# Performance work log

Measured on AMD Instinct MI355X. Metric: run time of the kernel, lower is better.

The kernel has to match this reference:

```python
import jax, jax.numpy as jnp
import numpy as np

N, D, DH, H = 2048, 256, 256, 4
DHEAD = DH // H
NEG = -1e30


def setup_inputs() -> dict:
    key = jax.random.key(0)
    ks = jax.random.split(key, 24)
    s = 0.05
    inp = {
        'axiom_states': jax.random.normal(ks[0], (N, D), jnp.float32),
        'adj0': (jax.random.uniform(ks[1], (N, N)) < 0.015).astype(jnp.float32),
        'adj1': (jax.random.uniform(ks[2], (N, N)) < 0.015).astype(jnp.float32),
        'w0': jax.random.uniform(ks[3], (N, N), jnp.float32),
        'w1': jax.random.uniform(ks[4], (N, N), jnp.float32),
        'Wm0': jax.random.normal(ks[5], (DH, D), jnp.float32) * s,
        'bm0': jax.random.normal(ks[6], (DH,), jnp.float32) * s,
        'Wa0': jax.random.normal(ks[7], (H, 2 * D), jnp.float32) * s,
        'ba0': jax.random.normal(ks[8], (H,), jnp.float32) * s,
        'Wm1': jax.random.normal(ks[9], (DH, D), jnp.float32) * s,
        'bm1': jax.random.normal(ks[10], (DH,), jnp.float32) * s,
        'Wa1': jax.random.normal(ks[11], (H, 2 * D), jnp.float32) * s,
        'ba1': jax.random.normal(ks[12], (H,), jnp.float32) * s,
        'gru_wih': jax.random.normal(ks[13], (3 * D, 2 * DH), jnp.float32) * s,
        'gru_whh': jax.random.normal(ks[14], (3 * D, D), jnp.float32) * s,
        'gru_bih': jax.random.normal(ks[15], (3 * D,), jnp.float32) * s,
        'gru_bhh': jax.random.normal(ks[16], (3 * D,), jnp.float32) * s,
        'ln_g': jnp.ones((D,), jnp.float32),
        'ln_b': jnp.zeros((D,), jnp.float32),
    }
    return inp


def _edge_messages(x, adj, w, Wm, bm, Wa, ba):
    # GAT-style decomposition of Linear([x_i, x_j]) -> a_cur[i] + a_nb[j] + b
    a_cur = x @ Wa[:, :D].T                      # [N,H] (target i, first half of concat)
    a_nb = x @ Wa[:, D:].T                       # [N,H] (neighbor j, second half)
    s = a_nb[:, None, :] + a_cur[None, :, :] + ba  # [j,i,H]
    s = jax.nn.leaky_relu(s, 0.2)
    s = s * w[:, :, None]                        # edge-weight scaled scores (pre-softmax)
    mask = adj != 0                              # edge j -> i iff adj[j,i] != 0
    logits = jnp.where(mask[:, :, None], s, NEG)
    attn = jax.nn.softmax(logits, axis=0) * mask[:, :, None]  # zero for isolated nodes
    msg = (x @ Wm.T + bm).reshape(N, H, DHEAD)   # per-neighbor messages
    agg = jnp.einsum('jih,jhd->ihd', attn, msg)  # softmax-weighted sum over neighbors
    return agg.reshape(N, DH)


def _forward(axiom_states, adj0, adj1, w0, w1, Wm0, bm0, Wa0, ba0,
             Wm1, bm1, Wa1, ba1, gru_wih, gru_whh, gru_bih, gru_bhh, ln_g, ln_b):
    m0 = _edge_messages(axiom_states, adj0, w0, Wm0, bm0, Wa0, ba0)
    m1 = _edge_messages(axiom_states, adj1, w1, Wm1, bm1, Wa1, ba1)
    msg = jnp.concatenate([m0, m1], axis=-1)     # dropout is identity in eval
    # GRUCell (torch semantics)
    gi = msg @ gru_wih.T + gru_bih
    gh = axiom_states @ gru_whh.T + gru_bhh
    r = jax.nn.sigmoid(gi[:, :D] + gh[:, :D])
    z = jax.nn.sigmoid(gi[:, D:2 * D] + gh[:, D:2 * D])
    n = jnp.tanh(gi[:, 2 * D:] + r * gh[:, 2 * D:])
    h = (1.0 - z) * n + z * axiom_states
    # LayerNorm
    mu = jnp.mean(h, axis=-1, keepdims=True)
    var = jnp.var(h, axis=-1, keepdims=True)
    return (h - mu) * jax.lax.rsqrt(var + 1e-5) * ln_g + ln_b


def reference(axiom_states, adj0, adj1, w0, w1, Wm0, bm0, Wa0, ba0,
              Wm1, bm1, Wa1, ba1, gru_wih, gru_whh, gru_bih, gru_bhh, ln_g, ln_b):
    return _forward(axiom_states, adj0, adj1, w0, w1, Wm0, bm0, Wa0, ba0,
                    Wm1, bm1, Wa1, ba1, gru_wih, gru_whh, gru_bih, gru_bhh, ln_g, ln_b)
```

## Files before the change

kernel.cpp:

```cpp
#include <hip/hip_runtime.h>

#define NN 2048
#define DD 256
#define HH 4
#define PW 1280
#define ECAP 128

typedef unsigned short ushort_t;
typedef __attribute__((ext_vector_type(4))) unsigned short us4;
typedef __attribute__((ext_vector_type(8))) short s8;
typedef __attribute__((ext_vector_type(4))) float f4;

__device__ __forceinline__ ushort_t f2b(float f) {
    unsigned int u = __float_as_uint(f);
    return (ushort_t)((u + 0x7fffu + ((u >> 16) & 1u)) >> 16);
}
__device__ __forceinline__ float b2f(ushort_t b) {
    return __uint_as_float(((unsigned int)b) << 16);
}
__device__ __forceinline__ void gl_lds16(const void* g, void* l) {
    __builtin_amdgcn_global_load_lds(
        (const __attribute__((address_space(1))) void*)g,
        (__attribute__((address_space(3))) void*)l, 16, 0, 0);
}

#define P_XC  512
#define P_WC  832
#define P_WI  1216
#define P_NB  1344

__global__ __launch_bounds__(256) void prep_kernel(
    const float* __restrict__ x,
    const float* __restrict__ Wm0, const float* __restrict__ Wm1,
    const float* __restrict__ whh, const float* __restrict__ wih,
    const float* __restrict__ Wa0, const float* __restrict__ Wa1,
    ushort_t* __restrict__ xb, ushort_t* __restrict__ Wcatb, ushort_t* __restrict__ wihb,
    float* __restrict__ acur, float* __restrict__ anb)
{
    __shared__ float sh[16][257];
    const int b = blockIdx.x, t = threadIdx.x;

    if (b < P_XC) {
        const int id = b * 1024 + t * 4;
        const float4 v = *(const float4*)(x + id);
        us4 o; o.x = f2b(v.x); o.y = f2b(v.y); o.z = f2b(v.z); o.w = f2b(v.w);
        *(us4*)(xb + id) = o;
        return;
    }
    if (b < P_WC) {
        const int id = (b - P_XC) * 1024 + t * 4;
        const int c = id >> 8, k = id & 255;
        const float* src = (c < 256) ? Wm0 + (size_t)c * DD + k
                         : (c < 512) ? Wm1 + (size_t)(c - 256) * DD + k
                                     : whh + (size_t)(c - 512) * DD + k;
        const float4 v = *(const float4*)src;
        us4 o; o.x = f2b(v.x); o.y = f2b(v.y); o.z = f2b(v.z); o.w = f2b(v.w);
        *(us4*)(Wcatb + id) = o;
        return;
    }
    if (b < P_WI) {
        const int id = (b - P_WC) * 1024 + t * 4;
        const float4 v = *(const float4*)(wih + id);
        us4 o; o.x = f2b(v.x); o.y = f2b(v.y); o.z = f2b(v.z); o.w = f2b(v.w);
        *(us4*)(wihb + id) = o;
        return;
    }
    {
        const int i0 = (b - P_WI) * 16;
        for (int rr = 0; rr < 16; ++rr)
            sh[rr][t] = x[(size_t)(i0 + rr) * DD + t];
        __syncthreads();
        const int r = t >> 4, idx = t & 15;
        const int l = idx >> 3, isnb = (idx >> 2) & 1, h = idx & 3;
        const float* wrow = (l ? Wa1 : Wa0) + h * (2 * DD) + isnb * DD;
        float acc = 0.f;
        for (int k = 0; k < DD; ++k) acc = fmaf(sh[r][k], wrow[k], acc);
        float* dst = isnb ? anb : acur;
        dst[((size_t)l * NN + i0 + r) * HH + h] = acc;
    }
}

__device__ __forceinline__ void gemm_core(
    const ushort_t* __restrict__ A, int lda, const ushort_t* __restrict__ B, int ldb,
    int r0, int c0, int K, ushort_t (*as)[64], ushort_t (*bs)[64], f4 acc[2][2])
{
    const int t = threadIdx.x;
    const int wave = t >> 6, lane = t & 63;
    const int wm = (wave & 1) * 32, wn = (wave >> 1) * 32;
    const int fm = lane & 15, fq = lane >> 4;

    const int m0q0 = wave * 16 + (lane >> 3);
    const int m0q1 = m0q0 + 8;
    const int cs0 = ((lane & 7) ^ (m0q0 & 7)) * 8;
    const int cs1 = ((lane & 7) ^ (m0q1 & 7)) * 8;
    const ushort_t* ga0 = A + (size_t)(r0 + m0q0) * lda + cs0;
    const ushort_t* ga1 = A + (size_t)(r0 + m0q1) * lda + cs1;
    const ushort_t* gb0 = B + (size_t)(c0 + m0q0) * ldb + cs0;
    const ushort_t* gb1 = B + (size_t)(c0 + m0q1) * ldb + cs1;
    ushort_t* la0 = &as[wave * 16][0];
    ushort_t* la1 = &as[wave * 16 + 8][0];
    ushort_t* lb0 = &bs[wave * 16][0];
    ushort_t* lb1 = &bs[wave * 16 + 8][0];
    const int ra0 = wm + fm, ra1 = wm + 16 + fm;
    const int rb0 = wn + fm, rb1 = wn + 16 + fm;

    for (int k0 = 0; k0 < K; k0 += 64) {
        __syncthreads();
        gl_lds16(ga0 + k0, la0);
        gl_lds16(ga1 + k0, la1);
        gl_lds16(gb0 + k0, lb0);
        gl_lds16(gb1 + k0, lb1);
        __syncthreads();
        #pragma unroll
        for (int kk = 0; kk < 2; ++kk) {
            const int cc = kk * 4 + fq;
            const s8 a0 = *(const s8*)&as[ra0][(cc ^ (ra0 & 7)) * 8];
            const s8 a1 = *(const s8*)&as[ra1][(cc ^ (ra1 & 7)) * 8];
            const s8 b0 = *(const s8*)&bs[rb0][(cc ^ (rb0 & 7)) * 8];
            const s8 b1 = *(const s8*)&bs[rb1][(cc ^ (rb1 & 7)) * 8];
            acc[0][0] = __builtin_amdgcn_mfma_f32_16x16x32_bf16(a0, b0, acc[0][0], 0, 0, 0);
            acc[0][1] = __builtin_amdgcn_mfma_f32_16x16x32_bf16(a0, b1, acc[0][1], 0, 0, 0);
            acc[1][0] = __builtin_amdgcn_mfma_f32_16x16x32_bf16(a1, b0, acc[1][0], 0, 0, 0);
            acc[1][1] = __builtin_amdgcn_mfma_f32_16x16x32_bf16(a1, b1, acc[1][1], 0, 0, 0);
        }
    }
}

__global__ __launch_bounds__(256) void gemm1_edge_kernel(
    const ushort_t* __restrict__ xb, const ushort_t* __restrict__ Wcatb,
    const float* __restrict__ bm0, const float* __restrict__ bm1,
    const float* __restrict__ bhh,
    ushort_t* __restrict__ msgb, float* __restrict__ gh,
    const float* __restrict__ adj0, const float* __restrict__ adj1,
    int* __restrict__ cnt, int* __restrict__ ej)
{
    __shared__ ushort_t as[64][64];
    __shared__ ushort_t bs[64][64];
    const int b = blockIdx.x, t = threadIdx.x;

    if (b < 640) {
        const int wave = t >> 6, lane = t & 63;
        const int wm = (wave & 1) * 32, wn = (wave >> 1) * 32;
        const int fm = lane & 15, fq = lane >> 4;
        const int c0 = (b % 20) * 64, r0 = (b / 20) * 64;
        f4 acc[2][2] = {};
        gemm_core(xb, DD, Wcatb, DD, r0, c0, DD, as, bs, acc);
        #pragma unroll
        for (int ni = 0; ni < 2; ++ni) {
            const int col = c0 + wn + ni * 16 + fm;
            const float bv = (col < 256) ? bm0[col]
                           : (col < 512) ? bm1[col - 256]
                                         : bhh[col - 512];
            #pragma unroll
            for (int mi = 0; mi < 2; ++mi) {
                #pragma unroll
                for (int r = 0; r < 4; ++r) {
                    const int row = r0 + wm + mi * 16 + fq * 4 + r;
                    const float v = acc[mi][ni][r] + bv;
                    if (col < 512) msgb[(size_t)row * 512 + col] = f2b(v);
                    else           gh[(size_t)row * 768 + col - 512] = v;
                }
            }
        }
        return;
    }
    {
        const int eb = b - 640;
        const int l = eb & 1, chunk = eb >> 1;
        const int i0 = chunk * 16;
        const float* adj = l ? adj1 : adj0;
        int* lcnt = (int*)as;
        if (t < 16) lcnt[t] = 0;
        __syncthreads();
        const int rowLane = t >> 2, q = t & 3;
        for (int r0r = 0; r0r < NN; r0r += 512) {
            float4 a[8];
            #pragma unroll
            for (int it = 0; it < 8; ++it) {
                const int j = r0r + it * 64 + rowLane;
                a[it] = *(const float4*)(adj + (size_t)j * NN + i0 + q * 4);
            }
            #pragma unroll
            for (int it = 0; it < 8; ++it) {
                const int j = r0r + it * 64 + rowLane;
                const float av[4] = {a[it].x, a[it].y, a[it].z, a[it].w};
                #pragma unroll
                for (int u = 0; u < 4; ++u) {
                    if (av[u] != 0.f) {
                        const int li = q * 4 + u;
                        const int slot = atomicAdd(&lcnt[li], 1);
                        if (slot < ECAP)
                            ej[((size_t)l * NN + i0 + li) * ECAP + slot] = j;
                    }
                }
            }
        }
        __syncthreads();
        if (t < 16) cnt[l * NN + i0 + t] = min(lcnt[t], ECAP);
    }
}

__global__ __launch_bounds__(256) void attn_kernel(
    const int* __restrict__ cnt, const int* __restrict__ ej,
    const float* __restrict__ w0, const float* __restrict__ w1,
    const float* __restrict__ acur, const float* __restrict__ anb,
    const float* __restrict__ ba0, const float* __restrict__ ba1,
    const ushort_t* __restrict__ msgb, ushort_t* __restrict__ mcatb)
{
    const int i = blockIdx.x, l = blockIdx.y, t = threadIdx.x;
    __shared__ float es[HH][ECAP];
    __shared__ int ejs[ECAP];
    const int ne = min(max(cnt[l * NN + i], 0), ECAP);
    const float* ba = l ? ba1 : ba0;
    const float* w  = l ? w1 : w0;
    const size_t ebase = ((size_t)l * NN + i) * ECAP;

    if (t < ne) {
        const int j = ej[ebase + t];
        const float wv = w[(size_t)j * NN + i];
        ejs[t] = j;
        const float4 av = *(const float4*)(anb + ((size_t)l * NN + j) * HH);
        const float sv[4] = {av.x, av.y, av.z, av.w};
        #pragma unroll
        for (int h = 0; h < HH; ++h) {
            float s = sv[h] + acur[((size_t)l * NN + i) * HH + h] + ba[h];
            s = (s > 0.f) ? s : 0.2f * s;
            es[h][t] = s * wv;
        }
    }
    __syncthreads();
    {
        const int h = t >> 6, lane = t & 63;
        float s0 = (lane < ne) ? es[h][lane] : -1e30f;
        float s1 = (lane + 64 < ne) ? es[h][lane + 64] : -1e30f;
        float m = fmaxf(s0, s1);
        #pragma unroll
        for (int off = 32; off; off >>= 1) m = fmaxf(m, __shfl_xor(m, off));
        const float p0 = expf(s0 - m), p1 = expf(s1 - m);
        float sum = p0 + p1;
        #pragma unroll
        for (int off = 32; off; off >>= 1) sum += __shfl_xor(sum, off);
        const float inv = (ne > 0) ? 1.f / sum : 0.f;
        es[h][lane] = p0 * inv;
        if (lane + 64 < ECAP) es[h][lane + 64] = p1 * inv;
    }
    __syncthreads();
    const int h = t >> 6;
    const int off = l * DD + t;
    float acc = 0.f;
    int e = 0;
    for (; e + 4 <= ne; e += 4) {
        const float v0 = b2f(msgb[(size_t)ejs[e + 0] * 512 + off]);
        const float v1 = b2f(msgb[(size_t)ejs[e + 1] * 512 + off]);
        const float v2 = b2f(msgb[(size_t)ejs[e + 2] * 512 + off]);
        const float v3 = b2f(msgb[(size_t)ejs[e + 3] * 512 + off]);
        acc = fmaf(es[h][e + 0], v0, acc);
        acc = fmaf(es[h][e + 1], v1, acc);
        acc = fmaf(es[h][e + 2], v2, acc);
        acc = fmaf(es[h][e + 3], v3, acc);
    }
    for (; e < ne; ++e)
        acc = fmaf(es[h][e], b2f(msgb[(size_t)ejs[e] * 512 + off]), acc);
    mcatb[(size_t)i * (2 * DD) + off] = f2b(acc);
}

__global__ __launch_bounds__(256) void gemm2_kernel(
    const ushort_t* __restrict__ mcatb, const ushort_t* __restrict__ wihb,
    const float* __restrict__ bih, float* __restrict__ gi)
{
    __shared__ ushort_t as[64][64];
    __shared__ ushort_t bs[64][64];
    const int t = threadIdx.x;
    const int wave = t >> 6, lane = t & 63;
    const int wm = (wave & 1) * 32, wn = (wave >> 1) * 32;
    const int fm = lane & 15, fq = lane >> 4;
    const int c0 = blockIdx.x * 64, r0 = blockIdx.y * 64;
    f4 acc[2][2] = {};
    gemm_core(mcatb, 512, wihb, 512, r0, c0, 512, as, bs, acc);
    #pragma unroll
    for (int ni = 0; ni < 2; ++ni) {
        const int col = c0 + wn + ni * 16 + fm;
        const float bv = bih[col];
        #pragma unroll
        for (int mi = 0; mi < 2; ++mi)
            #pragma unroll
            for (int r = 0; r < 4; ++r)
                gi[(size_t)(r0 + wm + mi * 16 + fq * 4 + r) * 768 + col] =
                    acc[mi][ni][r] + bv;
    }
}

__global__ __launch_bounds__(256) void gates_ln(
    const float* __restrict__ gi, const float* __restrict__ gh, const float* __restrict__ x,
    const float* __restrict__ lng, const float* __restrict__ lnb, float* __restrict__ out)
{
    __shared__ float rs1[4], rs2[4];
    const int t = threadIdx.x;
    const int r0 = blockIdx.x * 4;
    const float gv = lng[t], bv = lnb[t];
    float hv[4];
    #pragma unroll
    for (int r = 0; r < 4; ++r) {
        const int row = r0 + r;
        const float gir = gi[(size_t)row * 768 + t];
        const float giz = gi[(size_t)row * 768 + 256 + t];
        const float gin = gi[(size_t)row * 768 + 512 + t];
        const float ghr = gh[(size_t)row * 768 + t];
        const float ghz = gh[(size_t)row * 768 + 256 + t];
        const float ghn = gh[(size_t)row * 768 + 512 + t];
        const float rr = 1.f / (1.f + expf(-(gir + ghr)));
        const float zz = 1.f / (1.f + expf(-(giz + ghz)));
        const float nn = tanhf(gin + rr * ghn);
        hv[r] = (1.f - zz) * nn + zz * x[(size_t)row * DD + t];
    }
    const int lane = t & 63, wid = t >> 6;
    for (int r = 0; r < 4; ++r) {
        float s1 = hv[r], s2 = hv[r] * hv[r];
        #pragma unroll
        for (int off = 32; off; off >>= 1) {
            s1 += __shfl_down(s1, off);
            s2 += __shfl_down(s2, off);
        }
        if (lane == 0) { rs1[wid] = s1; rs2[wid] = s2; }
        __syncthreads();
        const float sum = rs1[0] + rs1[1] + rs1[2] + rs1[3];
        const float sq  = rs2[0] + rs2[1] + rs2[2] + rs2[3];
        const float mu  = sum * (1.f / DD);
        const float var = sq * (1.f / DD) - mu * mu;
        const float inv = rsqrtf(var + 1e-5f);
        out[(size_t)(r0 + r) * DD + t] = (hv[r] - mu) * inv * gv + bv;
        __syncthreads();
    }
}

extern "C" void kernel_launch(void* const* d_in, const int* in_sizes, int n_in,
                              void* d_out, int out_size, void* d_ws, size_t ws_size,
                              hipStream_t stream)
{
    const float* x    = (const float*)d_in[0];
    const float* adj0 = (const float*)d_in[1];
    const float* adj1 = (const float*)d_in[2];
    const float* w0   = (const float*)d_in[3];
    const float* w1   = (const float*)d_in[4];
    const float* Wm0  = (const float*)d_in[5];
    const float* bm0  = (const float*)d_in[6];
    const float* Wa0  = (const float*)d_in[7];
    const float* ba0  = (const float*)d_in[8];
    const float* Wm1  = (const float*)d_in[9];
    const float* bm1  = (const float*)d_in[10];
    const float* Wa1  = (const float*)d_in[11];
    const float* ba1  = (const float*)d_in[12];
    const float* wih  = (const float*)d_in[13];
    const float* whh  = (const float*)d_in[14];
    const float* bih  = (const float*)d_in[15];
    const float* bhh  = (const float*)d_in[16];
    const float* lng  = (const float*)d_in[17];
    const float* lnb  = (const float*)d_in[18];
    float* out = (float*)d_out;

    float* ws = (float*)d_ws;
    float* gh   = ws;            ws += (size_t)NN * 768;
    float* gi   = ws;            ws += (size_t)NN * 768;
    float* acur = ws;            ws += 2 * NN * HH;
    float* anb  = ws;            ws += 2 * NN * HH;
    int*   cnt  = (int*)ws;      ws += 2 * NN;
    int*   ej   = (int*)ws;      ws += 2 * NN * ECAP;
    ushort_t* xb    = (ushort_t*)ws;  ws += (size_t)NN * DD / 2;
    ushort_t* Wcatb = (ushort_t*)ws;  ws += (size_t)PW * DD / 2;
    ushort_t* wihb  = (ushort_t*)ws;  ws += (size_t)768 * 512 / 2;
    ushort_t* msgb  = (ushort_t*)ws;  ws += (size_t)NN * 512 / 2;
    ushort_t* mcatb = (ushort_t*)ws;  ws += (size_t)NN * 512 / 2;

    prep_kernel<<<P_NB, 256, 0, stream>>>(
        x, Wm0, Wm1, whh, wih, Wa0, Wa1, xb, Wcatb, wihb, acur, anb);
    gemm1_edge_kernel<<<896, 256, 0, stream>>>(
        xb, Wcatb, bm0, bm1, bhh, msgb, gh, adj0, adj1, cnt, ej);
    attn_kernel<<<dim3(NN, 2), 256, 0, stream>>>(
        cnt, ej, w0, w1, acur, anb, ba0, ba1, msgb, mcatb);
    gemm2_kernel<<<dim3(12, 32), 256, 0, stream>>>(mcatb, wihb, bih, gi);
    gates_ln<<<NN / 4, 256, 0, stream>>>(gi, gh, x, lng, lnb, out);
}
```

Measured before the change: 176.4 us.

## Fuse prep and first GEMM/edge kernels, converting fp32 to bf16 inside GEMM

Removes the separate prep kernel that converted x and the weights to bf16. The first GEMM now loads fp32 x and weights directly, converts them to bf16 in registers, and stores them to LDS. The adjacency scan, attention projections and wih conversion all move into one merged launch. This saves a kernel launch and the bf16 intermediate round-trip, at the cost of doubling global read bytes per GEMM tile and dropping the async global-to-LDS loads.

```diff
diff --git a/kernel.cpp b/kernel.cpp
--- a/kernel.cpp
+++ b/kernel.cpp
@@ -3,11 +3,11 @@
 #define NN 2048
 #define DD 256
 #define HH 4
-#define PW 1280
 #define ECAP 128
 
 typedef unsigned short ushort_t;
 typedef __attribute__((ext_vector_type(4))) unsigned short us4;
+typedef __attribute__((ext_vector_type(8))) unsigned short us8;
 typedef __attribute__((ext_vector_type(8))) short s8;
 typedef __attribute__((ext_vector_type(4))) float f4;
 
@@ -22,62 +22,6 @@
     __builtin_amdgcn_global_load_lds(
         (const __attribute__((address_space(1))) void*)g,
         (__attribute__((address_space(3))) void*)l, 16, 0, 0);
-}
-
-#define P_XC  512
-#define P_WC  832
-#define P_WI  1216
-#define P_NB  1344
-
-__global__ __launch_bounds__(256) void prep_kernel(
-    const float* __restrict__ x,
-    const float* __restrict__ Wm0, const float* __restrict__ Wm1,
-    const float* __restrict__ whh, const float* __restrict__ wih,
-    const float* __restrict__ Wa0, const float* __restrict__ Wa1,
-    ushort_t* __restrict__ xb, ushort_t* __restrict__ Wcatb, ushort_t* __restrict__ wihb,
-    float* __restrict__ acur, float* __restrict__ anb)
-{
-    __shared__ float sh[16][257];
-    const int b = blockIdx.x, t = threadIdx.x;
-
-    if (b < P_XC) {
-        const int id = b * 1024 + t * 4;
-        const float4 v = *(const float4*)(x + id);
-        us4 o; o.x = f2b(v.x); o.y = f2b(v.y); o.z = f2b(v.z); o.w = f2b(v.w);
-        *(us4*)(xb + id) = o;
-        return;
-    }
-    if (b < P_WC) {
-        const int id = (b - P_XC) * 1024 + t * 4;
-        const int c = id >> 8, k = id & 255;
-        const float* src = (c < 256) ? Wm0 + (size_t)c * DD + k
-                         : (c < 512) ? Wm1 + (size_t)(c - 256) * DD + k
-                                     : whh + (size_t)(c - 512) * DD + k;
-        const float4 v = *(const float4*)src;
-        us4 o; o.x = f2b(v.x); o.y = f2b(v.y); o.z = f2b(v.z); o.w = f2b(v.w);
-        *(us4*)(Wcatb + id) = o;
-        return;
-    }
-    if (b < P_WI) {
-        const int id = (b - P_WC) * 1024 + t * 4;
-        const float4 v = *(const float4*)(wih + id);
-        us4 o; o.x = f2b(v.x); o.y = f2b(v.y); o.z = f2b(v.z); o.w = f2b(v.w);
-        *(us4*)(wihb + id) = o;
-        return;
-    }
-    {
-        const int i0 = (b - P_WI) * 16;
-        for (int rr = 0; rr < 16; ++rr)
-            sh[rr][t] = x[(size_t)(i0 + rr) * DD + t];
-        __syncthreads();
-        const int r = t >> 4, idx = t & 15;
-        const int l = idx >> 3, isnb = (idx >> 2) & 1, h = idx & 3;
-        const float* wrow = (l ? Wa1 : Wa0) + h * (2 * DD) + isnb * DD;
-        float acc = 0.f;
-        for (int k = 0; k < DD; ++k) acc = fmaf(sh[r][k], wrow[k], acc);
-        float* dst = isnb ? anb : acur;
-        dst[((size_t)l * NN + i0 + r) * HH + h] = acc;
-    }
 }
 
 __device__ __forceinline__ void gemm_core(
@@ -126,50 +70,86 @@
     }
 }
 
-__global__ __launch_bounds__(256) void gemm1_edge_kernel(
-    const ushort_t* __restrict__ xb, const ushort_t* __restrict__ Wcatb,
+__device__ __forceinline__ us8 cvt8(float4 a, float4 b) {
+    us8 o;
+    o[0] = f2b(a.x); o[1] = f2b(a.y); o[2] = f2b(a.z); o[3] = f2b(a.w);
+    o[4] = f2b(b.x); o[5] = f2b(b.y); o[6] = f2b(b.z); o[7] = f2b(b.w);
+    return o;
+}
+
+__device__ __forceinline__ void gemm_core_f32(
+    const float* __restrict__ A, int lda, const float* __restrict__ B, int ldb,
+    int r0, int c0, int K, ushort_t (*as)[64], ushort_t (*bs)[64], f4 acc[2][2])
+{
+    const int t = threadIdx.x;
+    const int wave = t >> 6, lane = t & 63;
+    const int wm = (wave & 1) * 32, wn = (wave >> 1) * 32;
+    const int fm = lane & 15, fq = lane >> 4;
+
+    const int m1 = wave * 16 + (lane >> 3);
+    const int m2 = m1 + 8;
+    const int g1 = ((lane & 7) ^ (m1 & 7)) * 8;
+    const int g2 = ((lane & 7) ^ (m2 & 7)) * 8;
+    const int cl = (lane & 7) * 8;
+    const int ra0 = wm + fm, ra1 = wm + 16 + fm;
+    const int rb0 = wn + fm, rb1 = wn + 16 + fm;
+
+    for (int k0 = 0; k0 < K; k0 += 64) {
+        const float4 aa0 = *(const float4*)(A + (size_t)(r0 + m1) * lda + k0 + g1);
+        const float4 aa1 = *(const float4*)(A + (size_t)(r0 + m1) * lda + k0 + g1 + 4);
+        const float4 ab0 = *(const float4*)(A + (size_t)(r0 + m2) * lda + k0 + g2);
+        const float4 ab1 = *(const float4*)(A + (size_t)(r0 + m2) * lda + k0 + g2 + 4);
+        const float4 ba0 = *(const float4*)(B + (size_t)(c0 + m1) * ldb + k0 + g1);
+        const float4 ba1 = *(const float4*)(B + (size_t)(c0 + m1) * ldb + k0 + g1 + 4);
+        const float4 bb0 = *(const float4*)(B + (size_t)(c0 + m2) * ldb + k0 + g2);
+        const float4 bb1 = *(const float4*)(B + (size_t)(c0 + m2) * ldb + k0 + g2 + 4);
+        __syncthreads();
+        *(us8*)&as[m1][cl] = cvt8(aa0, aa1);
+        *(us8*)&as[m2][cl] = cvt8(ab0, ab1);
+        *(us8*)&bs[m1][cl] = cvt8(ba0, ba1);
+        *(us8*)&bs[m2][cl] = cvt8(bb0, bb1);
+        __syncthreads();
+        #pragma unroll
+        for (int kk = 0; kk < 2; ++kk) {
+            const int cc = kk * 4 + fq;
+            const s8 a0 = *(const s8*)&as[ra0][(cc ^ (ra0 & 7)) * 8];
+            const s8 a1 = *(const s8*)&as[ra1][(cc ^ (ra1 & 7)) * 8];
+            const s8 b0 = *(const s8*)&bs[rb0][(cc ^ (rb0 & 7)) * 8];
+            const s8 b1 = *(const s8*)&bs[rb1][(cc ^ (rb1 & 7)) * 8];
+            acc[0][0] = __builtin_amdgcn_mfma_f32_16x16x32_bf16(a0, b0, acc[0][0], 0, 0, 0);
+            acc[0][1] = __builtin_amdgcn_mfma_f32_16x16x32_bf16(a0, b1, acc[0][1], 0, 0, 0);
+            acc[1][0] = __builtin_amdgcn_mfma_f32_16x16x32_bf16(a1, b0, acc[1][0], 0, 0, 0);
+            acc[1][1] = __builtin_amdgcn_mfma_f32_16x16x32_bf16(a1, b1, acc[1][1], 0, 0, 0);
+        }
+    }
+}
+
+#define E_SC  256
+#define E_AP  384
+#define E_WI  768
+#define E_NB  1408
+
+__global__ __launch_bounds__(256) void fused1_kernel(
+    const float* __restrict__ x,
+    const float* __restrict__ adj0, const float* __restrict__ adj1,
+    const float* __restrict__ Wm0, const float* __restrict__ Wm1,
+    const float* __restrict__ whh, const float* __restrict__ wih,
+    const float* __restrict__ Wa0, const float* __restrict__ Wa1,
     const float* __restrict__ bm0, const float* __restrict__ bm1,
     const float* __restrict__ bhh,
-    ushort_t* __restrict__ msgb, float* __restrict__ gh,
-    const float* __restrict__ adj0, const float* __restrict__ adj1,
-    int* __restrict__ cnt, int* __restrict__ ej)
-{
-    __shared__ ushort_t as[64][64];
-    __shared__ ushort_t bs[64][64];
+    int* __restrict__ cnt, int* __restrict__ ej,
+    ushort_t* __restrict__ wihb,
+    float* __restrict__ acur, float* __restrict__ anb,
+    ushort_t* __restrict__ msgb, float* __restrict__ gh)
+{
+    __shared__ char smem[16448];
     const int b = blockIdx.x, t = threadIdx.x;
 
-    if (b < 640) {
-        const int wave = t >> 6, lane = t & 63;
-        const int wm = (wave & 1) * 32, wn = (wave >> 1) * 32;
-        const int fm = lane & 15, fq = lane >> 4;
-        const int c0 = (b % 20) * 64, r0 = (b / 20) * 64;
-        f4 acc[2][2] = {};
-        gemm_core(xb, DD, Wcatb, DD, r0, c0, DD, as, bs, acc);
-        #pragma unroll
-        for (int ni = 0; ni < 2; ++ni) {
-            const int col = c0 + wn + ni * 16 + fm;
-            const float bv = (col < 256) ? bm0[col]
-                           : (col < 512) ? bm1[col - 256]
-                                         : bhh[col - 512];
-            #pragma unroll
-            for (int mi = 0; mi < 2; ++mi) {
-                #pragma unroll
-                for (int r = 0; r < 4; ++r) {
-                    const int row = r0 + wm + mi * 16 + fq * 4 + r;
-                    const float v = acc[mi][ni][r] + bv;
-                    if (col < 512) msgb[(size_t)row * 512 + col] = f2b(v);
-                    else           gh[(size_t)row * 768 + col - 512] = v;
-                }
-            }
-        }
-        return;
-    }
-    {
-        const int eb = b - 640;
-        const int l = eb & 1, chunk = eb >> 1;
+    if (b < E_SC) {
+        const int l = b & 1, chunk = b >> 1;
         const int i0 = chunk * 16;
         const float* adj = l ? adj1 : adj0;
-        int* lcnt = (int*)as;
+        int* lcnt = (int*)smem;
         if (t < 16) lcnt[t] = 0;
         __syncthreads();
         const int rowLane = t >> 2, q = t & 3;
@@ -197,6 +177,60 @@
         }
         __syncthreads();
         if (t < 16) cnt[l * NN + i0 + t] = min(lcnt[t], ECAP);
+        return;
+    }
+    if (b < E_AP) {
+        float* sh = (float*)smem;
+        const int i0 = (b - E_SC) * 16;
+        for (int rr = 0; rr < 16; ++rr)
+            sh[rr * 257 + t] = x[(size_t)(i0 + rr) * DD + t];
+        __syncthreads();
+        const int r = t >> 4, idx = t & 15;
+        const int l = idx >> 3, isnb = (idx >> 2) & 1, h = idx & 3;
+        const float* wrow = (l ? Wa1 : Wa0) + h * (2 * DD) + isnb * DD;
+        float acc = 0.f;
+        for (int k = 0; k < DD; ++k) acc = fmaf(sh[r * 257 + k], wrow[k], acc);
+        float* dst = isnb ? anb : acur;
+        dst[((size_t)l * NN + i0 + r) * HH + h] = acc;
+        return;
+    }
+    if (b < E_WI) {
+        const int id = (b - E_AP) * 1024 + t * 4;
+        const float4 v = *(const float4*)(wih + id);
+        us4 o; o.x = f2b(v.x); o.y = f2b(v.y); o.z = f2b(v.z); o.w = f2b(v.w);
+        *(us4*)(wihb + id) = o;
+        return;
+    }
+    {
+        ushort_t (*as)[64] = (ushort_t(*)[64])smem;
+        ushort_t (*bs)[64] = (ushort_t(*)[64])(smem + 8192);
+        const int wave = t >> 6, lane = t & 63;
+        const int wm = (wave & 1) * 32, wn = (wave >> 1) * 32;
+        const int fm = lane & 15, fq = lane >> 4;
+        const int idx = b - E_WI;
+        const int c0 = (idx % 20) * 64, r0 = (idx / 20) * 64;
+        const float* Bsrc = (c0 < 256) ? Wm0 + (size_t)c0 * DD
+                          : (c0 < 512) ? Wm1 + (size_t)(c0 - 256) * DD
+                                       : whh + (size_t)(c0 - 512) * DD;
+        f4 acc[2][2] = {};
+        gemm_core_f32(x, DD, Bsrc, DD, r0, 0, DD, as, bs, acc);
+        #pragma unroll
+        for (int ni = 0; ni < 2; ++ni) {
+            const int col = c0 + wn + ni * 16 + fm;
+            const float bv = (col < 256) ? bm0[col]
+                           : (col < 512) ? bm1[col - 256]
+                                         : bhh[col - 512];
+            #pragma unroll
+            for (int mi = 0; mi < 2; ++mi) {
+                #pragma unroll
+                for (int r = 0; r < 4; ++r) {
+                    const int row = r0 + wm + mi * 16 + fq * 4 + r;
+                    const float v = acc[mi][ni][r] + bv;
+                    if (col < 512) msgb[(size_t)row * 512 + col] = f2b(v);
+                    else           gh[(size_t)row * 768 + col - 512] = v;
+                }
+            }
+        }
     }
 }
 
@@ -365,16 +399,13 @@
     float* anb  = ws;            ws += 2 * NN * HH;
     int*   cnt  = (int*)ws;      ws += 2 * NN;
     int*   ej   = (int*)ws;      ws += 2 * NN * ECAP;
-    ushort_t* xb    = (ushort_t*)ws;  ws += (size_t)NN * DD / 2;
-    ushort_t* Wcatb = (ushort_t*)ws;  ws += (size_t)PW * DD / 2;
     ushort_t* wihb  = (ushort_t*)ws;  ws += (size_t)768 * 512 / 2;
     ushort_t* msgb  = (ushort_t*)ws;  ws += (size_t)NN * 512 / 2;
     ushort_t* mcatb = (ushort_t*)ws;  ws += (size_t)NN * 512 / 2;
 
-    prep_kernel<<<P_NB, 256, 0, stream>>>(
-        x, Wm0, Wm1, whh, wih, Wa0, Wa1, xb, Wcatb, wihb, acur, anb);
-    gemm1_edge_kernel<<<896, 256, 0, stream>>>(
-        xb, Wcatb, bm0, bm1, bhh, msgb, gh, adj0, adj1, cnt, ej);
+    fused1_kernel<<<E_NB, 256, 0, stream>>>(
+        x, adj0, adj1, Wm0, Wm1, whh, wih, Wa0, Wa1, bm0, bm1, bhh,
+        cnt, ej, wihb, acur, anb, msgb, gh);
     attn_kernel<<<dim3(NN, 2), 256, 0, stream>>>(
         cnt, ej, w0, w1, acur, anb, ba0, ba1, msgb, mcatb);
     gemm2_kernel<<<dim3(12, 32), 256, 0, stream>>>(mcatb, wihb, bih, gi);
```

New measurement: 169.2 us (median of 2 runs). 4.1% less time.
